# Kernel optimization log

Measured on AMD Instinct MI355X. Metric: run time of the kernel, lower is better.

Reference implementation:

```python
import jax, jax.numpy as jnp
import numpy as np

N_NODES = 100000
N_EDGES = 3200000
N_IN = 128
N_HID = 128
N_OUT = 64
HOP = 10


def setup_inputs() -> dict:
    key = jax.random.key(0)
    ks = jax.random.split(key, 8)
    x = jax.random.normal(ks[0], (N_NODES, N_IN), dtype=jnp.float32)
    edge_row = jax.random.randint(ks[1], (N_EDGES,), 0, N_NODES, dtype=jnp.int32)
    edge_col = jax.random.randint(ks[2], (N_EDGES,), 0, N_NODES, dtype=jnp.int32)
    # normalized-ish edge weights so 10 hops of propagation stay bounded
    edge_val = jax.random.uniform(ks[3], (N_EDGES,), dtype=jnp.float32) / 32.0
    s_ih = 1.0 / np.sqrt(N_IN)
    s_hh = 1.0 / np.sqrt(N_HID)
    W_ih = jax.random.normal(ks[4], (4 * N_HID, N_IN), dtype=jnp.float32) * s_ih
    W_hh = jax.random.normal(ks[5], (4 * N_HID, N_HID), dtype=jnp.float32) * s_hh
    b_ih = jnp.zeros((4 * N_HID,), dtype=jnp.float32)
    b_hh = jnp.zeros((4 * N_HID,), dtype=jnp.float32)
    fc_w = jax.random.normal(ks[6], (N_OUT, N_HID), dtype=jnp.float32) * s_hh
    fc_b = jnp.zeros((N_OUT,), dtype=jnp.float32)
    return dict(x=x, edge_row=edge_row, edge_col=edge_col, edge_val=edge_val,
                W_ih=W_ih, W_hh=W_hh, b_ih=b_ih, b_hh=b_hh, fc_w=fc_w, fc_b=fc_b)


def _lstm_cell(x, h, c, W_ih, W_hh, b_ih, b_hh):
    # torch LSTMCell gate order: input, forget, cell(g), output
    gates = x @ W_ih.T + b_ih + h @ W_hh.T + b_hh  # [N, 4H]
    i, f, g, o = jnp.split(gates, 4, axis=-1)
    i = jax.nn.sigmoid(i)
    f = jax.nn.sigmoid(f)
    g = jnp.tanh(g)
    o = jax.nn.sigmoid(o)
    c_new = f * c + i * g
    h_new = o * jnp.tanh(c_new)
    return h_new, c_new


def _spmm(edge_row, edge_col, edge_val, h, n_nodes):
    # (A @ h)[r] = sum_{edges e with row r} val[e] * h[col[e]]
    msgs = edge_val[:, None] * h[edge_col]  # [E, H] gather
    return jax.ops.segment_sum(msgs, edge_row, num_segments=n_nodes)


def reference(x, edge_row, edge_col, edge_val, W_ih, W_hh, b_ih, b_hh, fc_w, fc_b):
    n = x.shape[0]
    h = jnp.zeros((n, W_hh.shape[1]), dtype=x.dtype)
    c = jnp.zeros_like(h)
    # hop iterations: LSTM gate update then sparse propagation (dropout = eval/identity)
    for _ in range(HOP):
        h, c = _lstm_cell(x, h, c, W_ih, W_hh, b_ih, b_hh)
        h = _spmm(edge_row, edge_col, edge_val, h, n)
    h = jax.nn.relu(h)
    return h @ fc_w.T + fc_b
```

## Files before the change

### kernel.cpp

```cpp
#include <hip/hip_runtime.h>
#include <hip/hip_bf16.h>
#include <math.h>

constexpr int NN  = 100000;
constexpr int EE  = 3200000;
constexpr int HID = 128;
constexpr int NG  = 512;
constexpr int NOUT = 64;
constexpr int HOPS = 10;
constexpr int SCAN_BLK = 1024;
constexpr int NBLK_SCAN = (NN + SCAN_BLK - 1) / SCAN_BLK;
constexpr int CELL_GRID = (NN + 63) / 64;
constexpr size_t CPERM_SLOTS = (size_t)CELL_GRID * 4 * 2 * 4 * 64;

typedef __attribute__((ext_vector_type(8))) short short8;
typedef __attribute__((ext_vector_type(4))) float f32x4;
typedef __attribute__((ext_vector_type(4))) _Float16 half4;
typedef unsigned long long ull;

__device__ __forceinline__ ushort f2bf(float f) {
    uint u = __builtin_bit_cast(uint, f);
    u += 0x7fff + ((u >> 16) & 1);
    return (ushort)(u >> 16);
}
__device__ __forceinline__ float bflo(uint u) { return __builtin_bit_cast(float, u << 16); }
__device__ __forceinline__ float bfhi(uint u) { return __builtin_bit_cast(float, u & 0xffff0000u); }

__device__ __forceinline__ float sigf(float v) { return 1.0f / (1.0f + __expf(-v)); }
__device__ __forceinline__ float tanh_fast(float x) {
    float t = __expf(-2.0f * fabsf(x));
    float r = (1.0f - t) / (1.0f + t);
    return copysignf(r, x);
}

__device__ __forceinline__ short8 load_frag(const ushort* p) {
    return *reinterpret_cast<const short8*>(p);
}
__device__ __forceinline__ f32x4 mfma16(short8 a, short8 b, f32x4 c) {
    return __builtin_amdgcn_mfma_f32_16x16x32_bf16(a, b, c, 0, 0, 0);
}

__global__ __launch_bounds__(256) void convert_bf16_kernel(
    const float* __restrict__ src, ushort* __restrict__ dst, int n4)
{
    int i = blockIdx.x * 256 + threadIdx.x;
    if (i < n4) {
        float4 v = reinterpret_cast<const float4*>(src)[i];
        ushort4 o;
        o.x = f2bf(v.x); o.y = f2bf(v.y); o.z = f2bf(v.z); o.w = f2bf(v.w);
        reinterpret_cast<ushort4*>(dst)[i] = o;
    }
}

__global__ __launch_bounds__(256) void bsum_kernel(
    const float* __restrict__ bih, const float* __restrict__ bhh, float* __restrict__ bsum)
{
    int i = blockIdx.x * 256 + threadIdx.x;
    if (i < NG) bsum[i] = bih[i] + bhh[i];
}

__global__ __launch_bounds__(256) void hist_kernel(const int* __restrict__ erow,
                                                   int* __restrict__ deg)
{
    int e = blockIdx.x * 256 + threadIdx.x;
    atomicAdd(&deg[erow[e]], 1);
}

__global__ __launch_bounds__(SCAN_BLK) void scan1_kernel(const int* __restrict__ deg,
                                                         int* __restrict__ bsums)
{
    __shared__ int tmp[SCAN_BLK];
    int t = threadIdx.x;
    int i = blockIdx.x * SCAN_BLK + t;
    tmp[t] = (i < NN) ? deg[i] : 0;
    __syncthreads();
    for (int off = SCAN_BLK / 2; off > 0; off >>= 1) {
        if (t < off) tmp[t] += tmp[t + off];
        __syncthreads();
    }
    if (t == 0) bsums[blockIdx.x] = tmp[0];
}

__global__ __launch_bounds__(128) void scan2_kernel(int* __restrict__ bsums)
{
    __shared__ int tmp[128];
    int t = threadIdx.x;
    tmp[t] = (t < NBLK_SCAN) ? bsums[t] : 0;
    __syncthreads();
    for (int off = 1; off < 128; off <<= 1) {
        int add = (t >= off) ? tmp[t - off] : 0;
        __syncthreads();
        tmp[t] += add;
        __syncthreads();
    }
    if (t < NBLK_SCAN) bsums[t] = (t == 0) ? 0 : tmp[t - 1];
}

__global__ __launch_bounds__(SCAN_BLK) void scan3_kernel(const int* __restrict__ deg,
                                                         const int* __restrict__ bsums,
                                                         int* __restrict__ rp,
                                                         int* __restrict__ cur)
{
    __shared__ int tmp[SCAN_BLK];
    int t = threadIdx.x;
    int i = blockIdx.x * SCAN_BLK + t;
    int v = (i < NN) ? deg[i] : 0;
    tmp[t] = v;
    __syncthreads();
    for (int off = 1; off < SCAN_BLK; off <<= 1) {
        int add = (t >= off) ? tmp[t - off] : 0;
        __syncthreads();
        tmp[t] += add;
        __syncthreads();
    }
    int incl = tmp[t] + bsums[blockIdx.x];
    if (i < NN) {
        rp[i + 1] = incl;
        cur[i] = incl - v;
    }
    if (i == 0) rp[0] = 0;
}

__global__ __launch_bounds__(256) void scatter_kernel(
    const int* __restrict__ erow, const int* __restrict__ ecol,
    const float* __restrict__ eval, int* __restrict__ cur,
    int2* __restrict__ epack)
{
    int e = blockIdx.x * 256 + threadIdx.x;
    int r = erow[e];
    int p = atomicAdd(&cur[r], 1);
    int2 pk;
    pk.x = ecol[e];
    pk.y = __builtin_bit_cast(int, eval[e]);
    epack[p] = pk;
}

template<bool FIRST>
__global__ __launch_bounds__(256, 2) void cell_kernel(
    const ushort* __restrict__ xb, const ushort* __restrict__ hb,
    const ushort* __restrict__ Wib, const ushort* __restrict__ Whb,
    const float* __restrict__ bsum, half4* __restrict__ cperm,
    ushort* __restrict__ hout)
{
    __shared__ __align__(16) ushort lds_h[64 * 136];

    const int t  = threadIdx.x;
    const int l  = t & 63;
    const int w  = t >> 6;
    const int lr = l & 15;
    const int lk = l >> 4;
    const int row0 = blockIdx.x * 64;

    f32x4 acc[8][4];
#pragma unroll
    for (int nI = 0; nI < 8; ++nI) {
        float b = bsum[(4 * nI + w) * 16 + lr];
#pragma unroll
        for (int rf = 0; rf < 4; ++rf) acc[nI][rf] = f32x4{b, b, b, b};
    }

    const short8 z8 = {0, 0, 0, 0, 0, 0, 0, 0};

    {
        short8 ax[4][4];
#pragma unroll
        for (int rf = 0; rf < 4; ++rf) {
            const int arow = row0 + rf * 16 + lr;
            const bool ok = arow < NN;
            const size_t ab = (size_t)arow * HID + lk * 8;
#pragma unroll
            for (int ks = 0; ks < 4; ++ks)
                ax[rf][ks] = ok ? load_frag(xb + ab + ks * 32) : z8;
        }
#pragma unroll
        for (int nI = 0; nI < 8; ++nI) {
            const int n = 4 * nI + w;
            const ushort* wip = Wib + (size_t)(n * 16 + lr) * HID + lk * 8;
            short8 bi[4];
#pragma unroll
            for (int ks = 0; ks < 4; ++ks) bi[ks] = load_frag(wip + ks * 32);
#pragma unroll
            for (int rf = 0; rf < 4; ++rf)
#pragma unroll
                for (int ks = 0; ks < 4; ++ks)
                    acc[nI][rf] = mfma16(ax[rf][ks], bi[ks], acc[nI][rf]);
        }
    }
    __builtin_amdgcn_sched_barrier(0);
    if (!FIRST) {
        short8 ah[4][4];
#pragma unroll
        for (int rf = 0; rf < 4; ++rf) {
            const int arow = row0 + rf * 16 + lr;
            const bool ok = arow < NN;
            const size_t ab = (size_t)arow * HID + lk * 8;
#pragma unroll
            for (int ks = 0; ks < 4; ++ks)
                ah[rf][ks] = ok ? load_frag(hb + ab + ks * 32) : z8;
        }
#pragma unroll
        for (int nI = 0; nI < 8; ++nI) {
            const int n = 4 * nI + w;
            const ushort* whp = Whb + (size_t)(n * 16 + lr) * HID + lk * 8;
            short8 bh[4];
#pragma unroll
            for (int ks = 0; ks < 4; ++ks) bh[ks] = load_frag(whp + ks * 32);
#pragma unroll
            for (int rf = 0; rf < 4; ++rf)
#pragma unroll
                for (int ks = 0; ks < 4; ++ks)
                    acc[nI][rf] = mfma16(ah[rf][ks], bh[ks], acc[nI][rf]);
        }
    }

#pragma unroll
    for (int nj = 0; nj < 2; ++nj) {
        const int col = (w + 4 * nj) * 16 + lr;
#pragma unroll
        for (int rf = 0; rf < 4; ++rf) {
            f32x4 iv = acc[nj][rf];
            f32x4 fv = acc[nj + 2][rf];
            f32x4 gv = acc[nj + 4][rf];
            f32x4 ov = acc[nj + 6][rf];
            const size_t cidx = ((((size_t)blockIdx.x * 4 + w) * 2 + nj) * 4 + rf) * 64 + l;
            float cold[4];
            if (FIRST) {
                cold[0] = cold[1] = cold[2] = cold[3] = 0.f;
            } else {
                half4 ch = cperm[cidx];
#pragma unroll
                for (int jj = 0; jj < 4; ++jj) cold[jj] = (float)ch[jj];
            }
            half4 cw;
            float hn[4];
#pragma unroll
            for (int jj = 0; jj < 4; ++jj) {
                float c2 = sigf(fv[jj]) * cold[jj] + sigf(iv[jj]) * tanh_fast(gv[jj]);
                cw[jj] = (_Float16)c2;
                hn[jj] = sigf(ov[jj]) * tanh_fast(c2);
            }
            cperm[cidx] = cw;
            const int rbase = rf * 16 + lk * 4;
#pragma unroll
            for (int jj = 0; jj < 4; ++jj)
                lds_h[(rbase + jj) * 136 + col] = f2bf(hn[jj]);
        }
    }
    __syncthreads();
    {
        const int trow = t >> 2;
        if (row0 + trow < NN) {
            const ushort* lsrc = &lds_h[trow * 136 + (t & 3) * 32];
            ushort* gdst = hout + (size_t)row0 * HID + t * 32;
#pragma unroll
            for (int j = 0; j < 4; ++j)
                *reinterpret_cast<short8*>(gdst + j * 8) =
                    *reinterpret_cast<const short8*>(lsrc + j * 8);
        }
    }
}

__global__ __launch_bounds__(256) void spmm_kernel(
    const int* __restrict__ rp, const int2* __restrict__ epack,
    const ushort* __restrict__ hin, ushort* __restrict__ hout)
{
    int r = blockIdx.x * 4 + (threadIdx.x >> 6);
    if (r >= NN) return;
    int l = threadIdx.x & 63;
    int beg = rp[r], end = rp[r + 1];
    const ull* eq = reinterpret_cast<const ull*>(epack);

    float s0a = 0.f, s1a = 0.f, s0b = 0.f, s1b = 0.f;
    float s0c = 0.f, s1c = 0.f, s0d = 0.f, s1d = 0.f;
    int e = beg;
    for (; e + 4 <= end; e += 4) {
        ull u0 = __builtin_nontemporal_load(eq + e);
        ull u1 = __builtin_nontemporal_load(eq + e + 1);
        ull u2 = __builtin_nontemporal_load(eq + e + 2);
        ull u3 = __builtin_nontemporal_load(eq + e + 3);
        int c0 = (int)(uint)u0, c1 = (int)(uint)u1, c2 = (int)(uint)u2, c3 = (int)(uint)u3;
        float v0 = __builtin_bit_cast(float, (uint)(u0 >> 32));
        float v1 = __builtin_bit_cast(float, (uint)(u1 >> 32));
        float v2 = __builtin_bit_cast(float, (uint)(u2 >> 32));
        float v3 = __builtin_bit_cast(float, (uint)(u3 >> 32));
        uint g0 = *reinterpret_cast<const uint*>(hin + (size_t)c0 * HID + l * 2);
        uint g1 = *reinterpret_cast<const uint*>(hin + (size_t)c1 * HID + l * 2);
        uint g2 = *reinterpret_cast<const uint*>(hin + (size_t)c2 * HID + l * 2);
        uint g3 = *reinterpret_cast<const uint*>(hin + (size_t)c3 * HID + l * 2);
        s0a += v0 * bflo(g0); s1a += v0 * bfhi(g0);
        s0b += v1 * bflo(g1); s1b += v1 * bfhi(g1);
        s0c += v2 * bflo(g2); s1c += v2 * bfhi(g2);
        s0d += v3 * bflo(g3); s1d += v3 * bfhi(g3);
    }
    for (; e < end; ++e) {
        ull u0 = __builtin_nontemporal_load(eq + e);
        int c0 = (int)(uint)u0;
        float v0 = __builtin_bit_cast(float, (uint)(u0 >> 32));
        uint g0 = *reinterpret_cast<const uint*>(hin + (size_t)c0 * HID + l * 2);
        s0a += v0 * bflo(g0); s1a += v0 * bfhi(g0);
    }
    float s0 = (s0a + s0b) + (s0c + s0d);
    float s1 = (s1a + s1b) + (s1c + s1d);
    uint o = ((uint)f2bf(s1) << 16) | (uint)f2bf(s0);
    *reinterpret_cast<uint*>(hout + (size_t)r * HID + l * 2) = o;
}

__global__ __launch_bounds__(256) void final_mfma_kernel(
    const ushort* __restrict__ hb, const ushort* __restrict__ fcwb,
    const float* __restrict__ fcb, float* __restrict__ out)
{
    const int t = threadIdx.x;
    const int l = t & 63;
    const int w = t >> 6;
    const int lr = l & 15;
    const int lk = l >> 4;
    const int row0 = blockIdx.x * 64 + w * 16;

    f32x4 acc[4];
#pragma unroll
    for (int n = 0; n < 4; ++n) {
        float b = fcb[n * 16 + lr];
        acc[n] = f32x4{b, b, b, b};
    }

    const short8 z8 = {0, 0, 0, 0, 0, 0, 0, 0};
    const int arow = row0 + lr;
    const bool aok = arow < NN;
    short8 a[4];
#pragma unroll
    for (int ks = 0; ks < 4; ++ks) {
        short8 v = aok ? load_frag(hb + (size_t)arow * HID + ks * 32 + lk * 8) : z8;
#pragma unroll
        for (int i = 0; i < 8; ++i) {
            ushort u = (ushort)v[i];
            if (u & 0x8000) v[i] = 0;
        }
        a[ks] = v;
    }

#pragma unroll
    for (int n = 0; n < 4; ++n) {
        const ushort* wp = fcwb + (size_t)(n * 16 + lr) * HID + lk * 8;
#pragma unroll
        for (int ks = 0; ks < 4; ++ks)
            acc[n] = mfma16(a[ks], load_frag(wp + ks * 32), acc[n]);
    }

#pragma unroll
    for (int n = 0; n < 4; ++n) {
#pragma unroll
        for (int j = 0; j < 4; ++j) {
            int row = row0 + lk * 4 + j;
            if (row < NN) out[(size_t)row * NOUT + n * 16 + lr] = acc[n][j];
        }
    }
}

extern "C" void kernel_launch(void* const* d_in, const int* in_sizes, int n_in,
                              void* d_out, int out_size, void* d_ws, size_t ws_size,
                              hipStream_t stream)
{
    const float* x    = (const float*)d_in[0];
    const int*   erow = (const int*)d_in[1];
    const int*   ecol = (const int*)d_in[2];
    const float* eval = (const float*)d_in[3];
    const float* Wih  = (const float*)d_in[4];
    const float* Whh  = (const float*)d_in[5];
    const float* bih  = (const float*)d_in[6];
    const float* bhh  = (const float*)d_in[7];
    const float* fcw  = (const float*)d_in[8];
    const float* fcb  = (const float*)d_in[9];
    float* out = (float*)d_out;

    char* ws = (char*)d_ws;
    size_t off = 0;
    auto alloc = [&](size_t bytes) -> void* {
        void* p = ws + off;
        off = (off + bytes + 255) & ~(size_t)255;
        return p;
    };
    ushort* hb_a  = (ushort*)alloc((size_t)NN * HID * 2);
    ushort* hb_b  = (ushort*)alloc((size_t)NN * HID * 2);
    half4*  cperm = (half4*)alloc(CPERM_SLOTS * 8);
    ushort* xb    = (ushort*)alloc((size_t)NN * HID * 2);
    ushort* Wib   = (ushort*)alloc((size_t)NG * HID * 2);
    ushort* Whb   = (ushort*)alloc((size_t)NG * HID * 2);
    ushort* fcwb  = (ushort*)alloc((size_t)NOUT * HID * 2);
    float*  bsum  = (float*)alloc((size_t)NG * 4);
    int*    rp    = (int*)alloc((size_t)(NN + 1) * 4);
    int*    deg   = (int*)alloc((size_t)NN * 4);
    int*    cur   = (int*)alloc((size_t)NN * 4);
    int*    bsums = (int*)alloc((size_t)NBLK_SCAN * 4);
    int2*   epack = (int2*)alloc((size_t)EE * 8);
    (void)ws_size;

    convert_bf16_kernel<<<(NN * HID / 4 + 255) / 256, 256, 0, stream>>>(x, xb, NN * HID / 4);
    convert_bf16_kernel<<<(NG * HID / 4 + 255) / 256, 256, 0, stream>>>(Wih, Wib, NG * HID / 4);
    convert_bf16_kernel<<<(NG * HID / 4 + 255) / 256, 256, 0, stream>>>(Whh, Whb, NG * HID / 4);
    convert_bf16_kernel<<<(NOUT * HID / 4 + 255) / 256, 256, 0, stream>>>(fcw, fcwb, NOUT * HID / 4);
    bsum_kernel<<<2, 256, 0, stream>>>(bih, bhh, bsum);

    hipMemsetAsync(deg, 0, (size_t)NN * 4, stream);
    hist_kernel<<<EE / 256, 256, 0, stream>>>(erow, deg);
    scan1_kernel<<<NBLK_SCAN, SCAN_BLK, 0, stream>>>(deg, bsums);
    scan2_kernel<<<1, 128, 0, stream>>>(bsums);
    scan3_kernel<<<NBLK_SCAN, SCAN_BLK, 0, stream>>>(deg, bsums, rp, cur);
    scatter_kernel<<<EE / 256, 256, 0, stream>>>(erow, ecol, eval, cur, epack);

    const int SPMM_GRID = NN / 4;

    cell_kernel<true><<<CELL_GRID, 256, 0, stream>>>(xb, hb_b, Wib, Whb, bsum, cperm, hb_a);
    spmm_kernel<<<SPMM_GRID, 256, 0, stream>>>(rp, epack, hb_a, hb_b);
    for (int hop = 1; hop < HOPS; ++hop) {
        cell_kernel<false><<<CELL_GRID, 256, 0, stream>>>(xb, hb_b, Wib, Whb, bsum, cperm, hb_a);
        spmm_kernel<<<SPMM_GRID, 256, 0, stream>>>(rp, epack, hb_a, hb_b);
    }

    final_mfma_kernel<<<(NN + 63) / 64, 256, 0, stream>>>(hb_b, fcwb, fcb, out);
}
```

Baseline: 2.990 ms.

## Make LSTM cell kernel persistent with register-resident gate weights

The cell kernel now runs a fixed grid of 256 blocks that loop over 32-row tiles. Each block loads the W_ih and W_hh fragments into registers once rather than re-reading them per 64-row tile. The aim is to remove repeated weight loads from global memory and cut per-block setup. In exchange register pressure rises sharply (launch bounds drop to one block per SM), there is only one wave per SIMD to hide x and h load latency, and 256 blocks may underfill the device.

```diff
diff --git a/kernel.cpp b/kernel.cpp
--- a/kernel.cpp
+++ b/kernel.cpp
@@ -10,8 +10,9 @@
 constexpr int HOPS = 10;
 constexpr int SCAN_BLK = 1024;
 constexpr int NBLK_SCAN = (NN + SCAN_BLK - 1) / SCAN_BLK;
-constexpr int CELL_GRID = (NN + 63) / 64;
-constexpr size_t CPERM_SLOTS = (size_t)CELL_GRID * 4 * 2 * 4 * 64;
+constexpr int NTILE = NN / 32;
+constexpr int PERSIST = 256;
+constexpr size_t CPERM_SLOTS = (size_t)NTILE * 4 * 2 * 2 * 64;
 
 typedef __attribute__((ext_vector_type(8))) short short8;
 typedef __attribute__((ext_vector_type(4))) float f32x4;
@@ -136,126 +137,118 @@
 }
 
 template<bool FIRST>
-__global__ __launch_bounds__(256, 2) void cell_kernel(
+__global__ __launch_bounds__(256, 1) void cell_kernel(
     const ushort* __restrict__ xb, const ushort* __restrict__ hb,
     const ushort* __restrict__ Wib, const ushort* __restrict__ Whb,
     const float* __restrict__ bsum, half4* __restrict__ cperm,
     ushort* __restrict__ hout)
 {
-    __shared__ __align__(16) ushort lds_h[64 * 136];
+    __shared__ __align__(16) ushort lds_h[32 * 136];
 
     const int t  = threadIdx.x;
     const int l  = t & 63;
     const int w  = t >> 6;
     const int lr = l & 15;
     const int lk = l >> 4;
-    const int row0 = blockIdx.x * 64;
-
-    f32x4 acc[8][4];
+
+    short8 wi[8][4], wh[8][4];
 #pragma unroll
     for (int nI = 0; nI < 8; ++nI) {
-        float b = bsum[(4 * nI + w) * 16 + lr];
-#pragma unroll
-        for (int rf = 0; rf < 4; ++rf) acc[nI][rf] = f32x4{b, b, b, b};
-    }
-
-    const short8 z8 = {0, 0, 0, 0, 0, 0, 0, 0};
-
-    {
-        short8 ax[4][4];
-#pragma unroll
-        for (int rf = 0; rf < 4; ++rf) {
-            const int arow = row0 + rf * 16 + lr;
-            const bool ok = arow < NN;
-            const size_t ab = (size_t)arow * HID + lk * 8;
-#pragma unroll
-            for (int ks = 0; ks < 4; ++ks)
-                ax[rf][ks] = ok ? load_frag(xb + ab + ks * 32) : z8;
-        }
+        const size_t wb = (size_t)((4 * nI + w) * 16 + lr) * HID + lk * 8;
+#pragma unroll
+        for (int ks = 0; ks < 4; ++ks) {
+            wi[nI][ks] = load_frag(Wib + wb + ks * 32);
+            if (!FIRST) wh[nI][ks] = load_frag(Whb + wb + ks * 32);
+        }
+    }
+    float bs[8];
+#pragma unroll
+    for (int nI = 0; nI < 8; ++nI) bs[nI] = bsum[(4 * nI + w) * 16 + lr];
+
+    for (int tile = blockIdx.x; tile < NTILE; tile += PERSIST) {
+        const int row0 = tile * 32;
+
+        f32x4 acc[8][2];
 #pragma unroll
         for (int nI = 0; nI < 8; ++nI) {
-            const int n = 4 * nI + w;
-            const ushort* wip = Wib + (size_t)(n * 16 + lr) * HID + lk * 8;
-            short8 bi[4];
-#pragma unroll
-            for (int ks = 0; ks < 4; ++ks) bi[ks] = load_frag(wip + ks * 32);
-#pragma unroll
-            for (int rf = 0; rf < 4; ++rf)
+            acc[nI][0] = f32x4{bs[nI], bs[nI], bs[nI], bs[nI]};
+            acc[nI][1] = acc[nI][0];
+        }
+
+        short8 a[2][4];
+#pragma unroll
+        for (int rf = 0; rf < 2; ++rf) {
+            const size_t ab = (size_t)(row0 + rf * 16 + lr) * HID + lk * 8;
+#pragma unroll
+            for (int ks = 0; ks < 4; ++ks) a[rf][ks] = load_frag(xb + ab + ks * 32);
+        }
+#pragma unroll
+        for (int nI = 0; nI < 8; ++nI)
+#pragma unroll
+            for (int rf = 0; rf < 2; ++rf)
 #pragma unroll
                 for (int ks = 0; ks < 4; ++ks)
-                    acc[nI][rf] = mfma16(ax[rf][ks], bi[ks], acc[nI][rf]);
-        }
-    }
-    __builtin_amdgcn_sched_barrier(0);
-    if (!FIRST) {
-        short8 ah[4][4];
-#pragma unroll
-        for (int rf = 0; rf < 4; ++rf) {
-            const int arow = row0 + rf * 16 + lr;
-            const bool ok = arow < NN;
-            const size_t ab = (size_t)arow * HID + lk * 8;
-#pragma unroll
-            for (int ks = 0; ks < 4; ++ks)
-                ah[rf][ks] = ok ? load_frag(hb + ab + ks * 32) : z8;
-        }
-#pragma unroll
-        for (int nI = 0; nI < 8; ++nI) {
-            const int n = 4 * nI + w;
-            const ushort* whp = Whb + (size_t)(n * 16 + lr) * HID + lk * 8;
-            short8 bh[4];
-#pragma unroll
-            for (int ks = 0; ks < 4; ++ks) bh[ks] = load_frag(whp + ks * 32);
-#pragma unroll
-            for (int rf = 0; rf < 4; ++rf)
-#pragma unroll
-                for (int ks = 0; ks < 4; ++ks)
-                    acc[nI][rf] = mfma16(ah[rf][ks], bh[ks], acc[nI][rf]);
-        }
-    }
-
-#pragma unroll
-    for (int nj = 0; nj < 2; ++nj) {
-        const int col = (w + 4 * nj) * 16 + lr;
-#pragma unroll
-        for (int rf = 0; rf < 4; ++rf) {
-            f32x4 iv = acc[nj][rf];
-            f32x4 fv = acc[nj + 2][rf];
-            f32x4 gv = acc[nj + 4][rf];
-            f32x4 ov = acc[nj + 6][rf];
-            const size_t cidx = ((((size_t)blockIdx.x * 4 + w) * 2 + nj) * 4 + rf) * 64 + l;
-            float cold[4];
-            if (FIRST) {
-                cold[0] = cold[1] = cold[2] = cold[3] = 0.f;
-            } else {
-                half4 ch = cperm[cidx];
-#pragma unroll
-                for (int jj = 0; jj < 4; ++jj) cold[jj] = (float)ch[jj];
+                    acc[nI][rf] = mfma16(a[rf][ks], wi[nI][ks], acc[nI][rf]);
+
+        if (!FIRST) {
+#pragma unroll
+            for (int rf = 0; rf < 2; ++rf) {
+                const size_t ab = (size_t)(row0 + rf * 16 + lr) * HID + lk * 8;
+#pragma unroll
+                for (int ks = 0; ks < 4; ++ks) a[rf][ks] = load_frag(hb + ab + ks * 32);
             }
-            half4 cw;
-            float hn[4];
-#pragma unroll
-            for (int jj = 0; jj < 4; ++jj) {
-                float c2 = sigf(fv[jj]) * cold[jj] + sigf(iv[jj]) * tanh_fast(gv[jj]);
-                cw[jj] = (_Float16)c2;
-                hn[jj] = sigf(ov[jj]) * tanh_fast(c2);
+#pragma unroll
+            for (int nI = 0; nI < 8; ++nI)
+#pragma unroll
+                for (int rf = 0; rf < 2; ++rf)
+#pragma unroll
+                    for (int ks = 0; ks < 4; ++ks)
+                        acc[nI][rf] = mfma16(a[rf][ks], wh[nI][ks], acc[nI][rf]);
+        }
+
+        __syncthreads();
+
+#pragma unroll
+        for (int nj = 0; nj < 2; ++nj) {
+            const int col = (w + 4 * nj) * 16 + lr;
+#pragma unroll
+            for (int rf = 0; rf < 2; ++rf) {
+                f32x4 iv = acc[nj][rf];
+                f32x4 fv = acc[nj + 2][rf];
+                f32x4 gv = acc[nj + 4][rf];
+                f32x4 ov = acc[nj + 6][rf];
+                const size_t cidx = ((((size_t)tile * 4 + w) * 2 + nj) * 2 + rf) * 64 + l;
+                float cold[4];
+                if (FIRST) {
+                    cold[0] = cold[1] = cold[2] = cold[3] = 0.f;
+                } else {
+                    half4 ch = cperm[cidx];
+#pragma unroll
+                    for (int jj = 0; jj < 4; ++jj) cold[jj] = (float)ch[jj];
+                }
+                half4 cw;
+                float hn[4];
+#pragma unroll
+                for (int jj = 0; jj < 4; ++jj) {
+                    float c2 = sigf(fv[jj]) * cold[jj] + sigf(iv[jj]) * tanh_fast(gv[jj]);
+                    cw[jj] = (_Float16)c2;
+                    hn[jj] = sigf(ov[jj]) * tanh_fast(c2);
+                }
+                cperm[cidx] = cw;
+                const int rbase = rf * 16 + lk * 4;
+#pragma unroll
+                for (int jj = 0; jj < 4; ++jj)
+                    lds_h[(rbase + jj) * 136 + col] = f2bf(hn[jj]);
             }
-            cperm[cidx] = cw;
-            const int rbase = rf * 16 + lk * 4;
-#pragma unroll
-            for (int jj = 0; jj < 4; ++jj)
-                lds_h[(rbase + jj) * 136 + col] = f2bf(hn[jj]);
-        }
-    }
-    __syncthreads();
-    {
-        const int trow = t >> 2;
-        if (row0 + trow < NN) {
-            const ushort* lsrc = &lds_h[trow * 136 + (t & 3) * 32];
-            ushort* gdst = hout + (size_t)row0 * HID + t * 32;
-#pragma unroll
-            for (int j = 0; j < 4; ++j)
-                *reinterpret_cast<short8*>(gdst + j * 8) =
-                    *reinterpret_cast<const short8*>(lsrc + j * 8);
+        }
+        __syncthreads();
+        {
+            const ushort* lsrc = &lds_h[(t >> 3) * 136 + (t & 7) * 16];
+            short8 v0 = *reinterpret_cast<const short8*>(lsrc);
+            short8 v1 = *reinterpret_cast<const short8*>(lsrc + 8);
+            ushort* gdst = hout + (size_t)row0 * HID + t * 16;
+            *reinterpret_cast<short8*>(gdst) = v0;
+            *reinterpret_cast<short8*>(gdst + 8) = v1;
         }
     }
 }
@@ -409,10 +402,10 @@
 
     const int SPMM_GRID = NN / 4;
 
-    cell_kernel<true><<<CELL_GRID, 256, 0, stream>>>(xb, hb_b, Wib, Whb, bsum, cperm, hb_a);
+    cell_kernel<true><<<PERSIST, 256, 0, stream>>>(xb, hb_b, Wib, Whb, bsum, cperm, hb_a);
     spmm_kernel<<<SPMM_GRID, 256, 0, stream>>>(rp, epack, hb_a, hb_b);
     for (int hop = 1; hop < HOPS; ++hop) {
-        cell_kernel<false><<<CELL_GRID, 256, 0, stream>>>(xb, hb_b, Wib, Whb, bsum, cperm, hb_a);
+        cell_kernel<false><<<PERSIST, 256, 0, stream>>>(xb, hb_b, Wib, Whb, bsum, cperm, hb_a);
         spmm_kernel<<<SPMM_GRID, 256, 0, stream>>>(rp, epack, hb_a, hb_b);
     }
 
```

Result: faster. 2.743 ms (-8.3%).
